# Kernel optimization log

Hardware: AMD Instinct MI355X
Metric: run time of the kernel (lower is better)

## Reference

```python
import jax, jax.numpy as jnp
import numpy as np

B, D = 65536, 784          # batch, input features
H = 256                     # delegator feature (hidden) dim
L = 64                      # num_leaves (experts)
C = 10                      # num_classes


def setup_inputs() -> dict:
    key = jax.random.key(0)
    ks = jax.random.split(key, 7)
    s_in = 1.0 / np.sqrt(D)
    s_h = 1.0 / np.sqrt(H)
    return {
        "x": jax.random.normal(ks[0], (B, D), dtype=jnp.float32),
        "Wf": jax.random.normal(ks[1], (D, H), dtype=jnp.float32) * s_in,   # Node feature proj
        "bf": jnp.zeros((H,), dtype=jnp.float32),
        "Wr": jax.random.normal(ks[2], (D, L), dtype=jnp.float32) * s_in,   # Node router proj
        "br": jnp.zeros((L,), dtype=jnp.float32),
        "Wl": jax.random.normal(ks[3], (L, H, C), dtype=jnp.float32) * s_h,  # per-leaf linear
        "bl": jnp.zeros((L, C), dtype=jnp.float32),
    }


def reference(x, Wf, bf, Wr, br, Wl, bl):
    # Delegator (Node): features + routing probabilities
    features = jax.nn.relu(x @ Wf + bf)                 # [B, H]
    probs = jax.nn.softmax(x @ Wr + br, axis=1)         # [B, L]
    choices = jnp.argmax(probs, axis=1)                 # [B] top-1 leaf per sample
    # Per-sample leaf dispatch: gather each sample's leaf weights, then a
    # batched vec-mat product (memory-bound gather, low FLOP/byte).
    Wc = Wl[choices]                                    # [B, H, C]
    bc = bl[choices]                                    # [B, C]
    predictions = jnp.einsum("bh,bhc->bc", features, Wc) + bc  # [B, C]
    return predictions
```

## Files before the change

kernel.cpp:

```cpp
#include <hip/hip_runtime.h>
#include <stdint.h>

#define B_ROWS 65536
#define D_IN   784
#define H_DIM  256
#define L_LEAF 64
#define C_CLS  10
#define N_COMB 320
#define K_PAD  832
#define BK     64
#define BM     64
#define NSTEP  13

#define GAP_THRESH 0.03f

using f32x4   = __attribute__((ext_vector_type(4))) float;
using bf16x8  = __attribute__((ext_vector_type(8))) short;
using ushort4v = __attribute__((ext_vector_type(4))) unsigned short;
using ushort8v = __attribute__((ext_vector_type(8))) unsigned short;

#define O_FLAGCNT  0
#define O_CHOICES  4096
#define O_FLAGROWS (4096 + 262144)
#define O_WT       (4096 + 262144 + 262144)
#define O_FEAT     (4096 + 262144 + 262144 + 532480)
#define WS_NEEDED  (O_FEAT + (size_t)B_ROWS * H_DIM * 2)

__device__ __forceinline__ unsigned short f2bf(float f) {
    union { float f; unsigned int u; } c; c.f = f;
    unsigned int u = c.u;
    return (unsigned short)((u + 0x7fffu + ((u >> 16) & 1u)) >> 16);
}
__device__ __forceinline__ float bf2f(unsigned short u) {
    union { unsigned int u; float f; } c; c.u = ((unsigned int)u) << 16;
    return c.f;
}

__global__ void k0_prep(const float* __restrict__ Wf, const float* __restrict__ Wr,
                        unsigned short* __restrict__ Wt, unsigned int* __restrict__ flagcnt) {
    if (blockIdx.x == 0 && threadIdx.x == 0) *flagcnt = 0u;
    __shared__ __align__(16) unsigned short tile[64 * 72];
    int bn = blockIdx.x % 5;
    int bk = blockIdx.x / 5;
    int t  = threadIdx.x;
    #pragma unroll
    for (int i = 0; i < 16; ++i) {
        int flat = i * 256 + t;
        int kk = flat >> 6, nn = flat & 63;
        int n = bn * 64 + nn;
        int k = bk * 64 + kk;
        float v = 0.f;
        if (k < D_IN) {
            v = (n < H_DIM) ? Wf[(size_t)k * H_DIM + n]
                            : Wr[(size_t)k * L_LEAF + (n - H_DIM)];
        }
        tile[nn * 72 + kk] = f2bf(v);
    }
    __syncthreads();
    #pragma unroll
    for (int i = 0; i < 2; ++i) {
        int flat = i * 256 + t;
        int nn = flat >> 3, kc = flat & 7;
        ushort8v v = *(const ushort8v*)(&tile[nn * 72 + kc * 8]);
        *(ushort8v*)(Wt + (size_t)(bn * 64 + nn) * K_PAD + bk * 64 + kc * 8) = v;
    }
}

__global__ __launch_bounds__(256, 2) void k1_gemm(
    const float* __restrict__ x, const unsigned short* __restrict__ Wt,
    const float* __restrict__ bfv, const float* __restrict__ brv,
    unsigned short* __restrict__ feat, int* __restrict__ choices,
    unsigned int* __restrict__ flagcnt, int* __restrict__ flagrows)
{
    __shared__ __align__(16) unsigned short Al[64 * 72];
    __shared__ __align__(16) unsigned short Bl[320 * 72];

    int t = threadIdx.x;
    int w = t >> 6, l = t & 63;
    int q = l >> 4, ic = l & 15;
    int bm0 = blockIdx.x * BM;
    int mrow0 = (w >> 1) * 32;
    int ncol0 = (w & 1) * 160;

    f32x4 acc[2][10];
    #pragma unroll
    for (int a = 0; a < 2; ++a)
        #pragma unroll
        for (int b = 0; b < 10; ++b)
            acc[a][b] = (f32x4){0.f, 0.f, 0.f, 0.f};

    for (int ts = 0; ts < NSTEP; ++ts) {
        int k0 = ts * BK;
        #pragma unroll
        for (int i = 0; i < 4; ++i) {
            int flat = i * 256 + t;
            int row = flat >> 4, kq = flat & 15;
            int kg = k0 + kq * 4;
            f32x4 v = (f32x4){0.f, 0.f, 0.f, 0.f};
            if (kg < D_IN) v = *(const f32x4*)(x + (size_t)(bm0 + row) * D_IN + kg);
            ushort4v h;
            h.x = f2bf(v.x); h.y = f2bf(v.y); h.z = f2bf(v.z); h.w = f2bf(v.w);
            *(ushort4v*)(&Al[row * 72 + kq * 4]) = h;
        }
        #pragma unroll
        for (int i = 0; i < 10; ++i) {
            int flat = i * 256 + t;
            int n = flat >> 3, kc = flat & 7;
            ushort8v v = *(const ushort8v*)(Wt + (size_t)n * K_PAD + k0 + kc * 8);
            *(ushort8v*)(&Bl[n * 72 + kc * 8]) = v;
        }
        __syncthreads();
        #pragma unroll
        for (int kk = 0; kk < 2; ++kk) {
            bf16x8 a0 = *(const bf16x8*)(&Al[(mrow0 +      ic) * 72 + kk * 32 + q * 8]);
            bf16x8 a1 = *(const bf16x8*)(&Al[(mrow0 + 16 + ic) * 72 + kk * 32 + q * 8]);
            #pragma unroll
            for (int nt = 0; nt < 10; ++nt) {
                bf16x8 b = *(const bf16x8*)(&Bl[(ncol0 + nt * 16 + ic) * 72 + kk * 32 + q * 8]);
                acc[0][nt] = __builtin_amdgcn_mfma_f32_16x16x32_bf16(a0, b, acc[0][nt], 0, 0, 0);
                acc[1][nt] = __builtin_amdgcn_mfma_f32_16x16x32_bf16(a1, b, acc[1][nt], 0, 0, 0);
            }
        }
        __syncthreads();
    }

    #pragma unroll
    for (int nt = 0; nt < 10; ++nt) {
        int col = ncol0 + nt * 16 + ic;
        if (col < H_DIM) {
            float bias = bfv[col];
            #pragma unroll
            for (int mt = 0; mt < 2; ++mt) {
                #pragma unroll
                for (int i = 0; i < 4; ++i) {
                    int row = bm0 + mrow0 + mt * 16 + q * 4 + i;
                    float v = acc[mt][nt][i] + bias;
                    v = v > 0.f ? v : 0.f;
                    feat[(size_t)row * H_DIM + col] = f2bf(v);
                }
            }
        }
    }

    if (ncol0 == 160) {
        #pragma unroll
        for (int mt = 0; mt < 2; ++mt) {
            #pragma unroll
            for (int i = 0; i < 4; ++i) {
                float m1 = -1e30f, m2 = -1e30f;
                int a1 = 0;
                #pragma unroll
                for (int nt = 6; nt < 10; ++nt) {
                    int leaf = (nt - 6) * 16 + ic;
                    float v = acc[mt][nt][i] + brv[leaf];
                    if (v > m1 || (v == m1 && leaf < a1)) { m2 = m1; m1 = v; a1 = leaf; }
                    else if (v > m2) { m2 = v; }
                }
                #pragma unroll
                for (int s = 1; s < 16; s <<= 1) {
                    float om1 = __shfl_xor(m1, s, 64);
                    float om2 = __shfl_xor(m2, s, 64);
                    int   oa1 = __shfl_xor(a1, s, 64);
                    bool take = (om1 > m1) || (om1 == m1 && oa1 < a1);
                    float nm2 = take ? fmaxf(om2, m1) : fmaxf(m2, om1);
                    m1 = take ? om1 : m1;
                    a1 = take ? oa1 : a1;
                    m2 = nm2;
                }
                if (ic == 0) {
                    int row = bm0 + mrow0 + mt * 16 + q * 4 + i;
                    choices[row] = a1;
                    if (m1 - m2 < GAP_THRESH) {
                        unsigned int idx = atomicAdd(flagcnt, 1u);
                        flagrows[idx] = row;
                    }
                }
            }
        }
    }
}

__global__ void k2_exact(const float* __restrict__ x, const float* __restrict__ Wr,
                         const float* __restrict__ brv,
                         const unsigned int* __restrict__ flagcnt,
                         const int* __restrict__ flagrows, int* __restrict__ choices)
{
    unsigned int cnt = *flagcnt;
    int l = threadIdx.x;
    for (unsigned int i = blockIdx.x; i < cnt; i += gridDim.x) {
        int row = flagrows[i];
        const float* xr = x + (size_t)row * D_IN;
        float s0 = 0.f, s1 = 0.f, s2 = 0.f, s3 = 0.f;
        for (int k = 0; k < D_IN; k += 4) {
            f32x4 xv = *(const f32x4*)(xr + k);
            s0 = fmaf(xv.x, Wr[(size_t)(k + 0) * L_LEAF + l], s0);
            s1 = fmaf(xv.y, Wr[(size_t)(k + 1) * L_LEAF + l], s1);
            s2 = fmaf(xv.z, Wr[(size_t)(k + 2) * L_LEAF + l], s2);
            s3 = fmaf(xv.w, Wr[(size_t)(k + 3) * L_LEAF + l], s3);
        }
        float v = (s0 + s1) + (s2 + s3) + brv[l];
        int a = l;
        #pragma unroll
        for (int s = 1; s < 64; s <<= 1) {
            float ov = __shfl_xor(v, s, 64);
            int   oa = __shfl_xor(a, s, 64);
            if (ov > v || (ov == v && oa < a)) { v = ov; a = oa; }
        }
        if (l == 0) choices[row] = a;
    }
}

__global__ __launch_bounds__(256) void k3_leaf(
    const unsigned short* __restrict__ feat, const int* __restrict__ choices,
    const float* __restrict__ Wl, const float* __restrict__ blv,
    float* __restrict__ out)
{
    int t = threadIdx.x;
    int wv = t >> 6, l = t & 63;
    int g = l >> 4, i = l & 15;
    int row = blockIdx.x * 16 + wv * 4 + g;
    int leaf = choices[row];

    ushort8v f0 = *(const ushort8v*)(feat + (size_t)row * H_DIM + i * 16);
    ushort8v f1 = *(const ushort8v*)(feat + (size_t)row * H_DIM + i * 16 + 8);
    float fv[16];
    #pragma unroll
    for (int j = 0; j < 8; ++j) { fv[j] = bf2f(f0[j]); fv[8 + j] = bf2f(f1[j]); }

    const float* wlb = Wl + (size_t)leaf * (H_DIM * C_CLS) + (size_t)i * 16 * C_CLS;
    float acc[C_CLS];
    #pragma unroll
    for (int c = 0; c < C_CLS; ++c) acc[c] = 0.f;
    #pragma unroll
    for (int h = 0; h < 16; ++h) {
        #pragma unroll
        for (int c = 0; c < C_CLS; ++c)
            acc[c] = fmaf(fv[h], wlb[h * C_CLS + c], acc[c]);
    }
    #pragma unroll
    for (int s = 1; s < 16; s <<= 1) {
        #pragma unroll
        for (int c = 0; c < C_CLS; ++c) acc[c] += __shfl_xor(acc[c], s, 64);
    }
    if (i == 0) {
        #pragma unroll
        for (int c = 0; c < C_CLS; ++c)
            out[(size_t)row * C_CLS + c] = acc[c] + blv[leaf * C_CLS + c];
    }
}

extern "C" void kernel_launch(void* const* d_in, const int* in_sizes, int n_in,
                              void* d_out, int out_size, void* d_ws, size_t ws_size,
                              hipStream_t stream) {
    if (ws_size < WS_NEEDED) return;

    const float* x   = (const float*)d_in[0];
    const float* Wf  = (const float*)d_in[1];
    const float* bfv = (const float*)d_in[2];
    const float* Wr  = (const float*)d_in[3];
    const float* brv = (const float*)d_in[4];
    const float* Wl  = (const float*)d_in[5];
    const float* blv = (const float*)d_in[6];
    float* out = (float*)d_out;

    char* ws = (char*)d_ws;
    unsigned int*   flagcnt  = (unsigned int*)(ws + O_FLAGCNT);
    int*            choices  = (int*)(ws + O_CHOICES);
    int*            flagrows = (int*)(ws + O_FLAGROWS);
    unsigned short* Wt       = (unsigned short*)(ws + O_WT);
    unsigned short* feat     = (unsigned short*)(ws + O_FEAT);

    hipLaunchKernelGGL(k0_prep, dim3(65), dim3(256), 0, stream, Wf, Wr, Wt, flagcnt);
    hipLaunchKernelGGL(k1_gemm, dim3(B_ROWS / BM), dim3(256), 0, stream,
                       x, Wt, bfv, brv, feat, choices, flagcnt, flagrows);
    hipLaunchKernelGGL(k2_exact, dim3(8192), dim3(64), 0, stream,
                       x, Wr, brv, flagcnt, flagrows, choices);
    hipLaunchKernelGGL(k3_leaf, dim3(B_ROWS / 16), dim3(256), 0, stream,
                       feat, choices, Wl, blv, out);
}
```

Before: 232.6 us.

## Double-buffer GEMM B tiles via direct global-to-LDS loads and bf16 leaf weights

Reworks the main GEMM so each wave owns 16 rows across all 320 output columns. The swizzled weight tiles are prefetched into a double-buffered LDS slot with direct global-to-LDS loads, and x is loaded straight into registers one step ahead, which removes the A-tile LDS staging. The weight prep kernel now writes a pre-swizzled per-step layout. The exact-routing fallback kernel stages Wr tiles in LDS and shares them across 4 flagged rows. Leaf weights are pre-converted to bf16 when workspace allows and loaded as vectors, which adds precision loss in the leaf product and more register pressure in the GEMM.

Result: faster. 195.0 us (-16.2%).

```diff
diff --git a/kernel.cpp b/kernel.cpp
--- a/kernel.cpp
+++ b/kernel.cpp
@@ -6,25 +6,23 @@
 #define H_DIM  256
 #define L_LEAF 64
 #define C_CLS  10
-#define N_COMB 320
-#define K_PAD  832
-#define BK     64
-#define BM     64
 #define NSTEP  13
-
+#define BTILE  40960
 #define GAP_THRESH 0.03f
 
-using f32x4   = __attribute__((ext_vector_type(4))) float;
-using bf16x8  = __attribute__((ext_vector_type(8))) short;
+using f32x4    = __attribute__((ext_vector_type(4))) float;
+using bf16x8   = __attribute__((ext_vector_type(8))) short;
+using ushort8v = __attribute__((ext_vector_type(8))) unsigned short;
 using ushort4v = __attribute__((ext_vector_type(4))) unsigned short;
-using ushort8v = __attribute__((ext_vector_type(8))) unsigned short;
 
 #define O_FLAGCNT  0
 #define O_CHOICES  4096
-#define O_FLAGROWS (4096 + 262144)
-#define O_WT       (4096 + 262144 + 262144)
-#define O_FEAT     (4096 + 262144 + 262144 + 532480)
-#define WS_NEEDED  (O_FEAT + (size_t)B_ROWS * H_DIM * 2)
+#define O_FLAGROWS (O_CHOICES + B_ROWS * 4)
+#define O_WT       (O_FLAGROWS + B_ROWS * 4)
+#define O_FEAT     (O_WT + NSTEP * BTILE)
+#define O_WLB      (O_FEAT + (size_t)B_ROWS * H_DIM * 2)
+#define WS_BASE    O_WLB
+#define WS_FULL    (O_WLB + (size_t)L_LEAF * H_DIM * C_CLS * 2)
 
 __device__ __forceinline__ unsigned short f2bf(float f) {
     union { float f; unsigned int u; } c; c.f = f;
@@ -36,34 +34,42 @@
     return c.f;
 }
 
+__device__ __forceinline__ void gload_lds16(const void* g, void* l) {
+    __builtin_amdgcn_global_load_lds(
+        (const __attribute__((address_space(1))) unsigned int*)g,
+        (__attribute__((address_space(3))) unsigned int*)l, 16, 0, 0);
+}
+
 __global__ void k0_prep(const float* __restrict__ Wf, const float* __restrict__ Wr,
                         unsigned short* __restrict__ Wt, unsigned int* __restrict__ flagcnt) {
     if (blockIdx.x == 0 && threadIdx.x == 0) *flagcnt = 0u;
-    __shared__ __align__(16) unsigned short tile[64 * 72];
-    int bn = blockIdx.x % 5;
-    int bk = blockIdx.x / 5;
-    int t  = threadIdx.x;
-    #pragma unroll
-    for (int i = 0; i < 16; ++i) {
-        int flat = i * 256 + t;
-        int kk = flat >> 6, nn = flat & 63;
-        int n = bn * 64 + nn;
-        int k = bk * 64 + kk;
-        float v = 0.f;
-        if (k < D_IN) {
-            v = (n < H_DIM) ? Wf[(size_t)k * H_DIM + n]
-                            : Wr[(size_t)k * L_LEAF + (n - H_DIM)];
-        }
-        tile[nn * 72 + kk] = f2bf(v);
-    }
-    __syncthreads();
-    #pragma unroll
-    for (int i = 0; i < 2; ++i) {
-        int flat = i * 256 + t;
-        int nn = flat >> 3, kc = flat & 7;
-        ushort8v v = *(const ushort8v*)(&tile[nn * 72 + kc * 8]);
-        *(ushort8v*)(Wt + (size_t)(bn * 64 + nn) * K_PAD + bk * 64 + kc * 8) = v;
-    }
+    const int ts = blockIdx.x;
+    const int t  = threadIdx.x;
+    #pragma unroll
+    for (int i = 0; i < 10; ++i) {
+        int id = i * 256 + t;
+        int n  = id % 320;
+        int c4 = id / 320;
+        int ks = ts * 64 + ((c4 ^ (n & 7)) << 3);
+        unsigned short v[8];
+        #pragma unroll
+        for (int j = 0; j < 8; ++j) {
+            int k = ks + j;
+            float f = 0.f;
+            if (k < D_IN)
+                f = (n < H_DIM) ? Wf[(size_t)k * H_DIM + n]
+                                : Wr[(size_t)k * L_LEAF + (n - H_DIM)];
+            v[j] = f2bf(f);
+        }
+        *(ushort8v*)((char*)Wt + (size_t)ts * BTILE + (size_t)(n * 8 + c4) * 16) = *(ushort8v*)v;
+    }
+}
+
+__global__ void k0b_wl(const float* __restrict__ Wl, unsigned short* __restrict__ Wlb) {
+    int i = (blockIdx.x * 256 + threadIdx.x) * 4;
+    f32x4 v = *(const f32x4*)(Wl + i);
+    ushort4v h; h.x = f2bf(v.x); h.y = f2bf(v.y); h.z = f2bf(v.z); h.w = f2bf(v.w);
+    *(ushort4v*)(Wlb + i) = h;
 }
 
 __global__ __launch_bounds__(256, 2) void k1_gemm(
@@ -72,154 +78,182 @@
     unsigned short* __restrict__ feat, int* __restrict__ choices,
     unsigned int* __restrict__ flagcnt, int* __restrict__ flagrows)
 {
-    __shared__ __align__(16) unsigned short Al[64 * 72];
-    __shared__ __align__(16) unsigned short Bl[320 * 72];
-
-    int t = threadIdx.x;
-    int w = t >> 6, l = t & 63;
-    int q = l >> 4, ic = l & 15;
-    int bm0 = blockIdx.x * BM;
-    int mrow0 = (w >> 1) * 32;
-    int ncol0 = (w & 1) * 160;
-
-    f32x4 acc[2][10];
-    #pragma unroll
-    for (int a = 0; a < 2; ++a)
-        #pragma unroll
-        for (int b = 0; b < 10; ++b)
-            acc[a][b] = (f32x4){0.f, 0.f, 0.f, 0.f};
-
+    __shared__ __align__(16) unsigned short Bl[2][320 * 64];
+
+    const int t = threadIdx.x, w = t >> 6, l = t & 63, q = l >> 4, ic = l & 15;
+    const int bm0 = blockIdx.x * 64;
+    const float* xrow = x + (size_t)(bm0 + w * 16 + ic) * D_IN;
+
+    f32x4 acc[20];
+    #pragma unroll
+    for (int i = 0; i < 20; ++i) acc[i] = (f32x4){0.f, 0.f, 0.f, 0.f};
+
+    const int rb0 = ic * 64 + (((q    ) ^ (ic & 7)) << 3);
+    const int rb1 = ic * 64 + (((q + 4) ^ (ic & 7)) << 3);
+
+    #pragma unroll
+    for (int i = 0; i < 10; ++i) {
+        int cid = i * 256 + t;
+        gload_lds16((const char*)Wt + cid * 16, (char*)&Bl[0][0] + cid * 16);
+    }
+    f32x4 an[4];
+    #pragma unroll
+    for (int kk = 0; kk < 2; ++kk) {
+        int kg = kk * 32 + q * 8;
+        an[2 * kk]     = *(const f32x4*)(xrow + kg);
+        an[2 * kk + 1] = *(const f32x4*)(xrow + kg + 4);
+    }
+    __syncthreads();
+
+    int cur = 0;
     for (int ts = 0; ts < NSTEP; ++ts) {
-        int k0 = ts * BK;
+        if (ts + 1 < NSTEP) {
+            const char* src = (const char*)Wt + (size_t)(ts + 1) * BTILE;
+            char* dst = (char*)&Bl[cur ^ 1][0];
+            #pragma unroll
+            for (int i = 0; i < 10; ++i) {
+                int cid = i * 256 + t;
+                gload_lds16(src + cid * 16, dst + cid * 16);
+            }
+        }
+        f32x4 ac0 = an[0], ac1 = an[1], ac2 = an[2], ac3 = an[3];
+        if (ts + 1 < NSTEP) {
+            #pragma unroll
+            for (int kk = 0; kk < 2; ++kk) {
+                int kg = (ts + 1) * 64 + kk * 32 + q * 8;
+                if (kg + 8 <= D_IN) {
+                    an[2 * kk]     = *(const f32x4*)(xrow + kg);
+                    an[2 * kk + 1] = *(const f32x4*)(xrow + kg + 4);
+                } else {
+                    an[2 * kk]     = (f32x4){0.f, 0.f, 0.f, 0.f};
+                    an[2 * kk + 1] = (f32x4){0.f, 0.f, 0.f, 0.f};
+                }
+            }
+        }
+        bf16x8 af0, af1;
+        #pragma unroll
+        for (int j = 0; j < 4; ++j) {
+            af0[j]     = (short)f2bf(ac0[j]);
+            af0[4 + j] = (short)f2bf(ac1[j]);
+            af1[j]     = (short)f2bf(ac2[j]);
+            af1[4 + j] = (short)f2bf(ac3[j]);
+        }
+        const unsigned short* Bc = &Bl[cur][0];
+        #pragma unroll
+        for (int nt = 0; nt < 20; ++nt) {
+            bf16x8 b = *(const bf16x8*)(Bc + nt * 1024 + rb0);
+            acc[nt] = __builtin_amdgcn_mfma_f32_16x16x32_bf16(af0, b, acc[nt], 0, 0, 0);
+        }
+        #pragma unroll
+        for (int nt = 0; nt < 20; ++nt) {
+            bf16x8 b = *(const bf16x8*)(Bc + nt * 1024 + rb1);
+            acc[nt] = __builtin_amdgcn_mfma_f32_16x16x32_bf16(af1, b, acc[nt], 0, 0, 0);
+        }
+        __syncthreads();
+        cur ^= 1;
+    }
+
+    #pragma unroll
+    for (int nt = 0; nt < 16; ++nt) {
+        int col = nt * 16 + ic;
+        float bias = bfv[col];
         #pragma unroll
         for (int i = 0; i < 4; ++i) {
-            int flat = i * 256 + t;
-            int row = flat >> 4, kq = flat & 15;
-            int kg = k0 + kq * 4;
-            f32x4 v = (f32x4){0.f, 0.f, 0.f, 0.f};
-            if (kg < D_IN) v = *(const f32x4*)(x + (size_t)(bm0 + row) * D_IN + kg);
-            ushort4v h;
-            h.x = f2bf(v.x); h.y = f2bf(v.y); h.z = f2bf(v.z); h.w = f2bf(v.w);
-            *(ushort4v*)(&Al[row * 72 + kq * 4]) = h;
-        }
-        #pragma unroll
-        for (int i = 0; i < 10; ++i) {
-            int flat = i * 256 + t;
-            int n = flat >> 3, kc = flat & 7;
-            ushort8v v = *(const ushort8v*)(Wt + (size_t)n * K_PAD + k0 + kc * 8);
-            *(ushort8v*)(&Bl[n * 72 + kc * 8]) = v;
-        }
-        __syncthreads();
-        #pragma unroll
-        for (int kk = 0; kk < 2; ++kk) {
-            bf16x8 a0 = *(const bf16x8*)(&Al[(mrow0 +      ic) * 72 + kk * 32 + q * 8]);
-            bf16x8 a1 = *(const bf16x8*)(&Al[(mrow0 + 16 + ic) * 72 + kk * 32 + q * 8]);
-            #pragma unroll
-            for (int nt = 0; nt < 10; ++nt) {
-                bf16x8 b = *(const bf16x8*)(&Bl[(ncol0 + nt * 16 + ic) * 72 + kk * 32 + q * 8]);
-                acc[0][nt] = __builtin_amdgcn_mfma_f32_16x16x32_bf16(a0, b, acc[0][nt], 0, 0, 0);
-                acc[1][nt] = __builtin_amdgcn_mfma_f32_16x16x32_bf16(a1, b, acc[1][nt], 0, 0, 0);
-            }
-        }
-        __syncthreads();
-    }
-
-    #pragma unroll
-    for (int nt = 0; nt < 10; ++nt) {
-        int col = ncol0 + nt * 16 + ic;
-        if (col < H_DIM) {
-            float bias = bfv[col];
-            #pragma unroll
-            for (int mt = 0; mt < 2; ++mt) {
-                #pragma unroll
-                for (int i = 0; i < 4; ++i) {
-                    int row = bm0 + mrow0 + mt * 16 + q * 4 + i;
-                    float v = acc[mt][nt][i] + bias;
-                    v = v > 0.f ? v : 0.f;
-                    feat[(size_t)row * H_DIM + col] = f2bf(v);
-                }
-            }
-        }
-    }
-
-    if (ncol0 == 160) {
-        #pragma unroll
-        for (int mt = 0; mt < 2; ++mt) {
-            #pragma unroll
-            for (int i = 0; i < 4; ++i) {
-                float m1 = -1e30f, m2 = -1e30f;
-                int a1 = 0;
-                #pragma unroll
-                for (int nt = 6; nt < 10; ++nt) {
-                    int leaf = (nt - 6) * 16 + ic;
-                    float v = acc[mt][nt][i] + brv[leaf];
-                    if (v > m1 || (v == m1 && leaf < a1)) { m2 = m1; m1 = v; a1 = leaf; }
-                    else if (v > m2) { m2 = v; }
-                }
-                #pragma unroll
-                for (int s = 1; s < 16; s <<= 1) {
-                    float om1 = __shfl_xor(m1, s, 64);
-                    float om2 = __shfl_xor(m2, s, 64);
-                    int   oa1 = __shfl_xor(a1, s, 64);
-                    bool take = (om1 > m1) || (om1 == m1 && oa1 < a1);
-                    float nm2 = take ? fmaxf(om2, m1) : fmaxf(m2, om1);
-                    m1 = take ? om1 : m1;
-                    a1 = take ? oa1 : a1;
-                    m2 = nm2;
-                }
-                if (ic == 0) {
-                    int row = bm0 + mrow0 + mt * 16 + q * 4 + i;
-                    choices[row] = a1;
-                    if (m1 - m2 < GAP_THRESH) {
-                        unsigned int idx = atomicAdd(flagcnt, 1u);
-                        flagrows[idx] = row;
-                    }
-                }
-            }
-        }
-    }
-}
-
-__global__ void k2_exact(const float* __restrict__ x, const float* __restrict__ Wr,
-                         const float* __restrict__ brv,
-                         const unsigned int* __restrict__ flagcnt,
-                         const int* __restrict__ flagrows, int* __restrict__ choices)
+            int row = bm0 + w * 16 + q * 4 + i;
+            float v = acc[nt][i] + bias;
+            v = v > 0.f ? v : 0.f;
+            feat[(size_t)row * H_DIM + col] = f2bf(v);
+        }
+    }
+    #pragma unroll
+    for (int i = 0; i < 4; ++i) {
+        float m1 = -1e30f, m2 = -1e30f;
+        int a1 = 0;
+        #pragma unroll
+        for (int nt = 16; nt < 20; ++nt) {
+            int leaf = (nt - 16) * 16 + ic;
+            float v = acc[nt][i] + brv[leaf];
+            if (v > m1) { m2 = m1; m1 = v; a1 = leaf; }
+            else if (v > m2) { m2 = v; }
+        }
+        #pragma unroll
+        for (int s = 1; s < 16; s <<= 1) {
+            float om1 = __shfl_xor(m1, s, 64);
+            float om2 = __shfl_xor(m2, s, 64);
+            int   oa1 = __shfl_xor(a1, s, 64);
+            bool take = (om1 > m1) || (om1 == m1 && oa1 < a1);
+            float nm2 = take ? fmaxf(om2, m1) : fmaxf(m2, om1);
+            m1 = take ? om1 : m1;
+            a1 = take ? oa1 : a1;
+            m2 = nm2;
+        }
+        if (ic == 0) {
+            int row = bm0 + w * 16 + q * 4 + i;
+            choices[row] = a1;
+            if (m1 - m2 < GAP_THRESH) {
+                unsigned int idx = atomicAdd(flagcnt, 1u);
+                flagrows[idx] = row;
+            }
+        }
+    }
+}
+
+__global__ __launch_bounds__(256) void k2_exact(
+    const float* __restrict__ x, const float* __restrict__ Wr,
+    const float* __restrict__ brv, const unsigned int* __restrict__ flagcnt,
+    const int* __restrict__ flagrows, int* __restrict__ choices)
 {
-    unsigned int cnt = *flagcnt;
-    int l = threadIdx.x;
-    for (unsigned int i = blockIdx.x; i < cnt; i += gridDim.x) {
-        int row = flagrows[i];
+    __shared__ float wl[64 * 64];
+    __shared__ float xl[4][64];
+    const unsigned int cnt = *flagcnt;
+    const int t = threadIdx.x, w = t >> 6, l = t & 63;
+    for (unsigned int base = blockIdx.x * 4u; base < cnt; base += gridDim.x * 4u) {
+        unsigned int ri = base + w;
+        int row = (ri < cnt) ? flagrows[ri] : 0;
         const float* xr = x + (size_t)row * D_IN;
         float s0 = 0.f, s1 = 0.f, s2 = 0.f, s3 = 0.f;
-        for (int k = 0; k < D_IN; k += 4) {
-            f32x4 xv = *(const f32x4*)(xr + k);
-            s0 = fmaf(xv.x, Wr[(size_t)(k + 0) * L_LEAF + l], s0);
-            s1 = fmaf(xv.y, Wr[(size_t)(k + 1) * L_LEAF + l], s1);
-            s2 = fmaf(xv.z, Wr[(size_t)(k + 2) * L_LEAF + l], s2);
-            s3 = fmaf(xv.w, Wr[(size_t)(k + 3) * L_LEAF + l], s3);
+        for (int kt = 0; kt < NSTEP; ++kt) {
+            int k0 = kt * 64;
+            #pragma unroll
+            for (int i = 0; i < 4; ++i) {
+                int flat = i * 256 + t;
+                int kk = flat >> 4, lq = (flat & 15) * 4;
+                int kg = k0 + kk;
+                f32x4 v = (f32x4){0.f, 0.f, 0.f, 0.f};
+                if (kg < D_IN) v = *(const f32x4*)(Wr + (size_t)kg * L_LEAF + lq);
+                *(f32x4*)&wl[kk * 64 + lq] = v;
+            }
+            xl[w][l] = (k0 + l < D_IN) ? xr[k0 + l] : 0.f;
+            __syncthreads();
+            #pragma unroll
+            for (int kk = 0; kk < 64; kk += 4) {
+                s0 = fmaf(xl[w][kk    ], wl[(kk    ) * 64 + l], s0);
+                s1 = fmaf(xl[w][kk + 1], wl[(kk + 1) * 64 + l], s1);
+                s2 = fmaf(xl[w][kk + 2], wl[(kk + 2) * 64 + l], s2);
+                s3 = fmaf(xl[w][kk + 3], wl[(kk + 3) * 64 + l], s3);
+            }
+            __syncthreads();
         }
         float v = (s0 + s1) + (s2 + s3) + brv[l];
         int a = l;
         #pragma unroll
-        for (int s = 1; s < 64; s <<= 1) {
-            float ov = __shfl_xor(v, s, 64);
-            int   oa = __shfl_xor(a, s, 64);
+        for (int st = 1; st < 64; st <<= 1) {
+            float ov = __shfl_xor(v, st, 64);
+            int   oa = __shfl_xor(a, st, 64);
             if (ov > v || (ov == v && oa < a)) { v = ov; a = oa; }
         }
-        if (l == 0) choices[row] = a;
+        if (l == 0 && ri < cnt) choices[row] = a;
     }
 }
 
 __global__ __launch_bounds__(256) void k3_leaf(
     const unsigned short* __restrict__ feat, const int* __restrict__ choices,
-    const float* __restrict__ Wl, const float* __restrict__ blv,
-    float* __restrict__ out)
+    const float* __restrict__ Wl, const unsigned short* __restrict__ Wlb,
+    const float* __restrict__ blv, float* __restrict__ out)
 {
-    int t = threadIdx.x;
-    int wv = t >> 6, l = t & 63;
-    int g = l >> 4, i = l & 15;
-    int row = blockIdx.x * 16 + wv * 4 + g;
-    int leaf = choices[row];
+    const int t = threadIdx.x, wv = t >> 6, l = t & 63, g = l >> 4, i = l & 15;
+    const int row = blockIdx.x * 16 + wv * 4 + g;
+    const int leaf = choices[row];
 
     ushort8v f0 = *(const ushort8v*)(feat + (size_t)row * H_DIM + i * 16);
     ushort8v f1 = *(const ushort8v*)(feat + (size_t)row * H_DIM + i * 16 + 8);
@@ -227,20 +261,36 @@
     #pragma unroll
     for (int j = 0; j < 8; ++j) { fv[j] = bf2f(f0[j]); fv[8 + j] = bf2f(f1[j]); }
 
-    const float* wlb = Wl + (size_t)leaf * (H_DIM * C_CLS) + (size_t)i * 16 * C_CLS;
     float acc[C_CLS];
     #pragma unroll
     for (int c = 0; c < C_CLS; ++c) acc[c] = 0.f;
-    #pragma unroll
-    for (int h = 0; h < 16; ++h) {
-        #pragma unroll
-        for (int c = 0; c < C_CLS; ++c)
-            acc[c] = fmaf(fv[h], wlb[h * C_CLS + c], acc[c]);
-    }
-    #pragma unroll
-    for (int s = 1; s < 16; s <<= 1) {
-        #pragma unroll
-        for (int c = 0; c < C_CLS; ++c) acc[c] += __shfl_xor(acc[c], s, 64);
+
+    if (Wlb) {
+        const unsigned short* wp = Wlb + ((size_t)leaf * H_DIM + i * 16) * C_CLS;
+        ushort8v wreg[20];
+        #pragma unroll
+        for (int j = 0; j < 20; ++j) wreg[j] = *(const ushort8v*)(wp + j * 8);
+        #pragma unroll
+        for (int h = 0; h < 16; ++h) {
+            #pragma unroll
+            for (int c = 0; c < C_CLS; ++c) {
+                int e = h * C_CLS + c;
+                acc[c] = fmaf(fv[h], bf2f(wreg[e >> 3][e & 7]), acc[c]);
+            }
+        }
+    } else {
+        const float* wp = Wl + ((size_t)leaf * H_DIM + i * 16) * C_CLS;
+        #pragma unroll
+        for (int h = 0; h < 16; ++h) {
+            #pragma unroll
+            for (int c = 0; c < C_CLS; ++c)
+                acc[c] = fmaf(fv[h], wp[h * C_CLS + c], acc[c]);
+        }
+    }
+    #pragma unroll
+    for (int st = 1; st < 16; st <<= 1) {
+        #pragma unroll
+        for (int c = 0; c < C_CLS; ++c) acc[c] += __shfl_xor(acc[c], st, 64);
     }
     if (i == 0) {
         #pragma unroll
@@ -252,7 +302,8 @@
 extern "C" void kernel_launch(void* const* d_in, const int* in_sizes, int n_in,
                               void* d_out, int out_size, void* d_ws, size_t ws_size,
                               hipStream_t stream) {
-    if (ws_size < WS_NEEDED) return;
+    if (ws_size < WS_BASE) return;
+    const bool use_bf = ws_size >= WS_FULL;
 
     const float* x   = (const float*)d_in[0];
     const float* Wf  = (const float*)d_in[1];
@@ -269,12 +320,15 @@
     int*            flagrows = (int*)(ws + O_FLAGROWS);
     unsigned short* Wt       = (unsigned short*)(ws + O_WT);
     unsigned short* feat     = (unsigned short*)(ws + O_FEAT);
-
-    hipLaunchKernelGGL(k0_prep, dim3(65), dim3(256), 0, stream, Wf, Wr, Wt, flagcnt);
-    hipLaunchKernelGGL(k1_gemm, dim3(B_ROWS / BM), dim3(256), 0, stream,
+    unsigned short* Wlb      = use_bf ? (unsigned short*)(ws + O_WLB) : (unsigned short*)0;
+
+    hipLaunchKernelGGL(k0_prep, dim3(NSTEP), dim3(256), 0, stream, Wf, Wr, Wt, flagcnt);
+    if (use_bf)
+        hipLaunchKernelGGL(k0b_wl, dim3(160), dim3(256), 0, stream, Wl, Wlb);
+    hipLaunchKernelGGL(k1_gemm, dim3(B_ROWS / 64), dim3(256), 0, stream,
                        x, Wt, bfv, brv, feat, choices, flagcnt, flagrows);
-    hipLaunchKernelGGL(k2_exact, dim3(8192), dim3(64), 0, stream,
+    hipLaunchKernelGGL(k2_exact, dim3(2048), dim3(256), 0, stream,
                        x, Wr, brv, flagcnt, flagrows, choices);
     hipLaunchKernelGGL(k3_leaf, dim3(B_ROWS / 16), dim3(256), 0, stream,
-                       feat, choices, Wl, blv, out);
-}
+                       feat, choices, Wl, Wlb, blv, out);
+}
```
